# Kernel optimization log

Hardware: AMD Instinct MI355X
Metric: run time of the kernel (lower is better)

Reference implementation:

```python
import jax, jax.numpy as jnp
import numpy as np

B, S, D, NH, HFF, VOCAB = 128, 100, 512, 8, 2048, 50000
DH = D // NH
GH, GL, NC = 256, 2, 10  # GRU hidden, GRU layers, num classes
NE = 3  # num encoders


def setup_inputs() -> dict:
    key = jax.random.key(0)
    ks = jax.random.split(key, 32)
    f = lambda k, shp, s=0.02: (jax.random.normal(k, shp, dtype=jnp.float32) * s)
    inp = {
        'x': jax.random.randint(ks[0], (B, S), 0, VOCAB),
        'x1': jnp.ones((B, S), dtype=jnp.float32),
        'emb': f(ks[1], (VOCAB, D)),
        'Wq': f(ks[2], (NE, D, D)), 'bq': jnp.zeros((NE, D)),
        'Wk': f(ks[3], (NE, D, D)), 'bk': jnp.zeros((NE, D)),
        'Wv': f(ks[4], (NE, D, D)), 'bv': jnp.zeros((NE, D)),
        'Wo': f(ks[5], (NE, D, D)), 'bo': jnp.zeros((NE, D)),
        'g1': jnp.ones((NE, D)), 'be1': jnp.zeros((NE, D)),
        'W1': f(ks[6], (NE, D, HFF)), 'b1': jnp.zeros((NE, HFF)),
        'W2': f(ks[7], (NE, HFF, D)), 'b2': jnp.zeros((NE, D)),
        'g2': jnp.ones((NE, D)), 'be2': jnp.zeros((NE, D)),
        'gru_Wih': f(ks[8], (GL, 2, 3 * GH, D)),
        'gru_Whh': f(ks[9], (GL, 2, 3 * GH, GH)),
        'gru_bih': jnp.zeros((GL, 2, 3 * GH)),
        'gru_bhh': jnp.zeros((GL, 2, 3 * GH)),
        'fc_W': f(ks[10], (2 * GH + D, NC)), 'fc_b': jnp.zeros((NC,)),
    }
    return inp


def _layer_norm(x, g, b, eps=1e-5):
    m = jnp.mean(x, axis=-1, keepdims=True)
    v = jnp.mean((x - m) ** 2, axis=-1, keepdims=True)
    return (x - m) / jnp.sqrt(v + eps) * g + b


def _forward(x, emb, Wq, bq, Wk, bk, Wv, bv, Wo, bo, g1, be1, W1, b1, W2, b2,
             g2, be2, gru_Wih, gru_Whh, gru_bih, gru_bhh, fc_W, fc_b):
    out = emb[x]  # [B, S, D]
    scale = DH ** -0.5
    for l in range(NE):
        # NOTE: torch code uses a contiguous view(B*NH, -1, DH), not a
        # transpose-based head split; plain reshape reproduces it exactly.
        Q = (out @ Wq[l] + bq[l]).reshape(B * NH, S, DH)
        K = (out @ Wk[l] + bk[l]).reshape(B * NH, S, DH)
        V = (out @ Wv[l] + bv[l]).reshape(B * NH, S, DH)
        att = jax.nn.softmax(jnp.einsum('bqd,bkd->bqk', Q, K) * scale, axis=-1)
        ctx = (att @ V).reshape(B, S, D)
        out = _layer_norm(ctx @ Wo[l] + bo[l] + out, g1[l], be1[l])
        ff = jnp.maximum(out @ W1[l] + b1[l], 0.0) @ W2[l] + b2[l]
        out = _layer_norm(ff + out, g2[l], be2[l])
    embed_feat = out

    # Bidirectional multi-layer GRU (torch cuDNN formulation), seq-major.
    h_seq = jnp.transpose(out, (1, 0, 2))  # [S, B, D]
    for l in range(GL):
        dirs = []
        for d in range(2):
            Wih, Whh = gru_Wih[l, d], gru_Whh[l, d]
            bih, bhh = gru_bih[l, d], gru_bhh[l, d]
            xp = h_seq @ Wih.T + bih  # [S, B, 3H]

            def step(h, xpt, Whh=Whh, bhh=bhh):
                hp = h @ Whh.T + bhh
                r = jax.nn.sigmoid(xpt[:, :GH] + hp[:, :GH])
                z = jax.nn.sigmoid(xpt[:, GH:2 * GH] + hp[:, GH:2 * GH])
                n = jnp.tanh(xpt[:, 2 * GH:] + r * hp[:, 2 * GH:])
                hn = (1.0 - z) * n + z * h
                return hn, hn

            h0 = jnp.zeros((B, GH), dtype=h_seq.dtype)
            _, ys = jax.lax.scan(step, h0, xp, reverse=(d == 1))
            dirs.append(ys)
        h_seq = jnp.concatenate(dirs, axis=-1)  # [S, B, 2H]
    gru_out = jnp.transpose(h_seq, (1, 0, 2))  # [B, S, 2H]

    feat = jnp.maximum(jnp.concatenate([embed_feat, gru_out], axis=-1), 0.0)
    pooled = jnp.max(feat, axis=1)  # MaxPool1d(pad_size) over seq -> [B, 2H+D]
    return pooled @ fc_W + fc_b


def reference(x, x1, emb, Wq, bq, Wk, bk, Wv, bv, Wo, bo, g1, be1, W1, b1,
              W2, b2, g2, be2, gru_Wih, gru_Whh, gru_bih, gru_bhh, fc_W, fc_b):
    # x1 (mask) is dead in the original module: the masked attention result is
    # immediately overwritten by the unmasked call, so it does not affect output.
    return _forward(x, emb, Wq, bq, Wk, bk, Wv, bv, Wo, bo, g1, be1, W1, b1,
                    W2, b2, g2, be2, gru_Wih, gru_Whh, gru_bih, gru_bhh,
                    fc_W, fc_b)
```

## Files before the change

kernel.cpp:

```cpp
#include <hip/hip_runtime.h>
#include <cstdint>

typedef __bf16 bf16x8 __attribute__((ext_vector_type(8)));
typedef float f32x4 __attribute__((ext_vector_type(4)));
typedef unsigned short ushort8 __attribute__((ext_vector_type(8)));

#define DEV __device__ __forceinline__
#define MFMA16(a, b, c) __builtin_amdgcn_mfma_f32_16x16x32_bf16((a), (b), (c), 0, 0, 0)
#define MFMA_AG(acc, hf, wf) \
  asm("v_mfma_f32_16x16x32_bf16 %0, %1, %2, %0" : "+v"(acc) : "v"(hf), "a"(wf))

DEV unsigned short f2b(float x) {
  union { float f; unsigned int u; } c; c.f = x;
  unsigned int u = c.u + 0x7fffu + ((c.u >> 16) & 1u);
  return (unsigned short)(u >> 16);
}
DEV float b2f(unsigned short x) {
  union { unsigned int u; float f; } c; c.u = ((unsigned int)x) << 16;
  return c.f;
}
DEV void gld_lds16(const void* g, void* l) {
  __builtin_amdgcn_global_load_lds(
      (const __attribute__((address_space(1))) unsigned int*)(uintptr_t)g,
      (__attribute__((address_space(3))) unsigned int*)(uintptr_t)l, 16, 0, 0);
}

__global__ __launch_bounds__(256) void convT_k(const float* __restrict__ in,
                                               unsigned short* __restrict__ out,
                                               int K, int N) {
  __shared__ float tile[64][65];
  int k0 = blockIdx.x * 64, n0 = blockIdx.y * 64;
  int wv = threadIdx.x >> 6, ln = threadIdx.x & 63;
  #pragma unroll
  for (int i = 0; i < 16; ++i) {
    int r = wv * 16 + i;
    tile[r][ln] = in[(size_t)(k0 + r) * N + (n0 + ln)];
  }
  __syncthreads();
  #pragma unroll
  for (int i = 0; i < 16; ++i) {
    int r = wv * 16 + i;
    out[(size_t)(n0 + r) * K + (k0 + ln)] = f2b(tile[ln][r]);
  }
}

__global__ void convB_k(const float* __restrict__ in, unsigned short* __restrict__ out, int n) {
  int stride = gridDim.x * blockDim.x;
  for (int i = blockIdx.x * blockDim.x + threadIdx.x; i < n; i += stride)
    out[i] = f2b(in[i]);
}

__global__ __launch_bounds__(256) void biasC_k(const float* __restrict__ bih,
                                               const float* __restrict__ bhh,
                                               float* __restrict__ cb) {
  int i = blockIdx.x * 256 + threadIdx.x;
  if (i < 4 * 768) {
    int c = i % 768;
    cb[i] = bih[i] + (c < 512 ? bhh[i] : 0.f);
  }
}

__global__ __launch_bounds__(256) void embed_k(const int* __restrict__ x, const float* __restrict__ emb,
                                               float* __restrict__ cf, unsigned short* __restrict__ cb) {
  int row = blockIdx.x * 4 + (threadIdx.x >> 6);
  int lane = threadIdx.x & 63;
  int tok = x[row];
  const float4* src = (const float4*)(emb + (size_t)tok * 512 + lane * 8);
  float4 a = src[0], b = src[1];
  float4* dst = (float4*)(cf + (size_t)row * 512 + lane * 8);
  dst[0] = a; dst[1] = b;
  ushort8 pk;
  pk[0] = f2b(a.x); pk[1] = f2b(a.y); pk[2] = f2b(a.z); pk[3] = f2b(a.w);
  pk[4] = f2b(b.x); pk[5] = f2b(b.y); pk[6] = f2b(b.z); pk[7] = f2b(b.w);
  *(ushort8*)(cb + (size_t)row * 512 + lane * 8) = pk;
}

DEV void stage_tile(const unsigned short* g, int ld, unsigned short* lds, int lane, int wave) {
  #pragma unroll
  for (int i = 0; i < 2; ++i) {
    int r0 = (i * 4 + wave) * 16;
    const unsigned short* src = g + (size_t)(r0 + (lane >> 2)) * ld + (lane & 3) * 8;
    gld_lds16(src, lds + r0 * 32);
  }
}

template <int RELU, int RES, int OF32, int OB16>
__global__ __launch_bounds__(256) void gemm_k(
    const unsigned short* __restrict__ A, const unsigned short* __restrict__ BT,
    const float* __restrict__ bias, const float* __restrict__ res,
    float* __restrict__ Cf, unsigned short* __restrict__ Cb,
    int M, int N, int K) {
  __shared__ unsigned short sA[2][128 * 32];
  __shared__ unsigned short sB[2][128 * 32];
  int tid = threadIdx.x, lane = tid & 63, wave = tid >> 6;
  int m0 = blockIdx.x * 128, n0 = blockIdx.y * 128;
  int lm = lane & 15, lk = (lane >> 4) * 8;
  int wr = wave >> 1, wc = wave & 1;
  f32x4 acc[4][4];
  #pragma unroll
  for (int i = 0; i < 4; ++i)
    #pragma unroll
    for (int j = 0; j < 4; ++j) acc[i][j] = (f32x4){0.f, 0.f, 0.f, 0.f};
  const unsigned short* Ab = A + (size_t)m0 * K;
  const unsigned short* Bb = BT + (size_t)n0 * K;
  int nk = K >> 5;
  stage_tile(Ab, K, sA[0], lane, wave);
  stage_tile(Bb, K, sB[0], lane, wave);
  __syncthreads();
  int buf = 0;
  for (int t = 0; t < nk; ++t) {
    if (t + 1 < nk) {
      stage_tile(Ab + (t + 1) * 32, K, sA[buf ^ 1], lane, wave);
      stage_tile(Bb + (t + 1) * 32, K, sB[buf ^ 1], lane, wave);
    }
    bf16x8 aF[4], bF[4];
    #pragma unroll
    for (int i = 0; i < 4; ++i) aF[i] = *(const bf16x8*)&sA[buf][(wr * 64 + i * 16 + lm) * 32 + lk];
    #pragma unroll
    for (int j = 0; j < 4; ++j) bF[j] = *(const bf16x8*)&sB[buf][(wc * 64 + j * 16 + lm) * 32 + lk];
    #pragma unroll
    for (int i = 0; i < 4; ++i)
      #pragma unroll
      for (int j = 0; j < 4; ++j) acc[i][j] = MFMA16(aF[i], bF[j], acc[i][j]);
    __syncthreads();
    buf ^= 1;
  }
  #pragma unroll
  for (int i = 0; i < 4; ++i) {
    int gr0 = m0 + wr * 64 + i * 16 + (lane >> 4) * 4;
    #pragma unroll
    for (int j = 0; j < 4; ++j) {
      int gc = n0 + wc * 64 + j * 16 + lm;
      float bv = bias[gc];
      #pragma unroll
      for (int q = 0; q < 4; ++q) {
        size_t idx = (size_t)(gr0 + q) * N + gc;
        float v = acc[i][j][q] + bv;
        if (RES) v += res[idx];
        if (RELU) v = fmaxf(v, 0.f);
        if (OF32) Cf[idx] = v;
        if (OB16) Cb[idx] = f2b(v);
      }
    }
  }
}

__global__ __launch_bounds__(256) void attn_k(const unsigned short* __restrict__ Q,
                                              const unsigned short* __restrict__ Kv,
                                              const unsigned short* __restrict__ V,
                                              unsigned short* __restrict__ ctx) {
  __shared__ unsigned short Ks[112 * 64];
  __shared__ unsigned short VT[64 * 128];
  __shared__ unsigned short Ps[112 * 128];
  int g = blockIdx.x;
  size_t base = (size_t)g * 6400;
  int tid = threadIdx.x, lane = tid & 63, wave = tid >> 6;
  int lm = lane & 15, lg = lane >> 4, lk = lg * 8;
  for (int idx = tid; idx < 112 * 8; idx += 256) {
    int row = idx >> 3, c8 = (idx & 7) * 8;
    int rr = row < 100 ? row : 99;
    *(ushort8*)&Ks[row * 64 + c8] = *(const ushort8*)&Kv[base + (size_t)rr * 64 + c8];
  }
  for (int idx = tid; idx < 64 * 28; idx += 256) { int c = idx / 28, j = idx % 28; VT[c * 128 + 100 + j] = 0; }
  for (int idx = tid; idx < 112 * 16; idx += 256) { int r = idx / 16, c = idx % 16; Ps[r * 128 + 112 + c] = 0; }
  for (int idx = tid; idx < 6400; idx += 256) {
    int c = idx / 100, j = idx % 100;
    VT[c * 128 + j] = V[base + (size_t)j * 64 + c];
  }
  __syncthreads();
  for (int rt = wave; rt < 7; rt += 4) {
    int arow = rt * 16 + lm;
    int qrow = arow < 100 ? arow : 99;
    bf16x8 aF0 = *(const bf16x8*)&Q[base + (size_t)qrow * 64 + lk];
    bf16x8 aF1 = *(const bf16x8*)&Q[base + (size_t)qrow * 64 + 32 + lk];
    f32x4 sc[7];
    #pragma unroll
    for (int ct = 0; ct < 7; ++ct) {
      bf16x8 b0 = *(const bf16x8*)&Ks[(ct * 16 + lm) * 64 + lk];
      bf16x8 b1 = *(const bf16x8*)&Ks[(ct * 16 + lm) * 64 + 32 + lk];
      f32x4 a = {0.f, 0.f, 0.f, 0.f};
      a = MFMA16(aF0, b0, a);
      a = MFMA16(aF1, b1, a);
      sc[ct] = a;
    }
    #pragma unroll
    for (int q = 0; q < 4; ++q) {
      float mx = -1e30f;
      #pragma unroll
      for (int ct = 0; ct < 7; ++ct) {
        int col = ct * 16 + lm;
        float v = sc[ct][q] * 0.125f;
        if (col < 100) mx = fmaxf(mx, v);
      }
      for (int off = 1; off < 16; off <<= 1) mx = fmaxf(mx, __shfl_xor(mx, off));
      float sum = 0.f; float pv[7];
      #pragma unroll
      for (int ct = 0; ct < 7; ++ct) {
        int col = ct * 16 + lm;
        float e = (col < 100) ? __expf(sc[ct][q] * 0.125f - mx) : 0.f;
        pv[ct] = e; sum += e;
      }
      for (int off = 1; off < 16; off <<= 1) sum += __shfl_xor(sum, off);
      float inv = 1.f / sum;
      int prow = rt * 16 + lg * 4 + q;
      #pragma unroll
      for (int ct = 0; ct < 7; ++ct) Ps[prow * 128 + ct * 16 + lm] = f2b(pv[ct] * inv);
    }
  }
  __syncthreads();
  for (int rt = wave; rt < 7; rt += 4) {
    bf16x8 aP[4];
    #pragma unroll
    for (int kc = 0; kc < 4; ++kc) aP[kc] = *(const bf16x8*)&Ps[(rt * 16 + lm) * 128 + kc * 32 + lk];
    #pragma unroll
    for (int ctp = 0; ctp < 4; ++ctp) {
      f32x4 o = {0.f, 0.f, 0.f, 0.f};
      #pragma unroll
      for (int kc = 0; kc < 4; ++kc) {
        bf16x8 bV = *(const bf16x8*)&VT[(ctp * 16 + lm) * 128 + kc * 32 + lk];
        o = MFMA16(aP[kc], bV, o);
      }
      #pragma unroll
      for (int q = 0; q < 4; ++q) {
        int ri = rt * 16 + lg * 4 + q;
        if (ri < 100) ctx[base + (size_t)ri * 64 + ctp * 16 + lm] = f2b(o[q]);
      }
    }
  }
}

__global__ __launch_bounds__(256) void ln_k(const float* __restrict__ in, const float* __restrict__ gamma,
                                            const float* __restrict__ beta, float* __restrict__ outF,
                                            unsigned short* __restrict__ outB) {
  int row = blockIdx.x * 4 + (threadIdx.x >> 6);
  int lane = threadIdx.x & 63;
  const float* p = in + (size_t)row * 512 + lane * 8;
  float4 v0 = *(const float4*)p;
  float4 v1 = *(const float4*)(p + 4);
  float x[8] = {v0.x, v0.y, v0.z, v0.w, v1.x, v1.y, v1.z, v1.w};
  float s = 0.f;
  #pragma unroll
  for (int e = 0; e < 8; ++e) s += x[e];
  #pragma unroll
  for (int off = 1; off < 64; off <<= 1) s += __shfl_xor(s, off);
  float mean = s * (1.f / 512.f);
  float vs = 0.f;
  #pragma unroll
  for (int e = 0; e < 8; ++e) { float d = x[e] - mean; vs += d * d; }
  #pragma unroll
  for (int off = 1; off < 64; off <<= 1) vs += __shfl_xor(vs, off);
  float rstd = rsqrtf(vs * (1.f / 512.f) + 1e-5f);
  int c0 = lane * 8;
  ushort8 pk;
  #pragma unroll
  for (int e = 0; e < 8; ++e) {
    float y = (x[e] - mean) * rstd * gamma[c0 + e] + beta[c0 + e];
    x[e] = y; pk[e] = f2b(y);
  }
  float4* po = (float4*)(outF + (size_t)row * 512 + c0);
  po[0] = make_float4(x[0], x[1], x[2], x[3]);
  po[1] = make_float4(x[4], x[5], x[6], x[7]);
  *(ushort8*)(outB + (size_t)row * 512 + c0) = pk;
}

__global__ __launch_bounds__(128) void seqT_k(const unsigned short* __restrict__ in,
                                              unsigned short* __restrict__ out) {
  int o = blockIdx.x;
  int s = o >> 7, b = o & 127;
  const uint2* src = (const uint2*)(in + (size_t)(b * 100 + s) * 512);
  uint2* dst = (uint2*)(out + (size_t)o * 512);
  dst[threadIdx.x] = src[threadIdx.x];
}

__global__ __launch_bounds__(512) __attribute__((amdgpu_waves_per_eu(2, 2))) void gru_k(
    const unsigned short* __restrict__ WhhB,
    const float* __restrict__ bhh,
    const float* __restrict__ xp,
    unsigned short* __restrict__ hout)
{
  __shared__ unsigned short hb[2][16 * 256];
  __shared__ char ldsn[131072];
  const int dir = blockIdx.x >> 3, bsl = blockIdx.x & 7;
  const int tid = threadIdx.x, lane = tid & 63, w = tid >> 6;
  const int lm = lane & 15, lg = lane >> 4, lk = lg * 8;
  const int col = w * 32 + lm;

  for (int i = tid; i < 16 * 256; i += 512) hb[0][i] = 0;

  {
    const unsigned short* wn = WhhB + (size_t)(dir * 768 + 512) * 256;
    #pragma unroll
    for (int ct = 0; ct < 2; ++ct)
      #pragma unroll
      for (int kt = 0; kt < 8; ++kt) {
        const unsigned short* src = wn + (size_t)(w * 32 + lm + ct * 16) * 256 + kt * 32 + lk;
        gld_lds16(src, ldsn + ((w * 2 + ct) * 8 + kt) * 1024);
      }
  }

  bf16x8 wr[2][8], wz[2][8];
  #pragma unroll
  for (int ct = 0; ct < 2; ++ct) {
    const unsigned short* wpr = WhhB + (size_t)(dir * 768 + col + ct * 16) * 256;
    const unsigned short* wpz = WhhB + (size_t)(dir * 768 + 256 + col + ct * 16) * 256;
    #pragma unroll
    for (int kt = 0; kt < 8; ++kt) {
      wr[ct][kt] = *(const bf16x8*)&wpr[kt * 32 + lk];
      wz[ct][kt] = *(const bf16x8*)&wpz[kt * 32 + lk];
    }
  }
  #pragma unroll
  for (int ct = 0; ct < 2; ++ct)
    #pragma unroll
    for (int kt = 0; kt < 8; ++kt) {
      asm("" : "+a"(wr[ct][kt]));
      asm("" : "+a"(wz[ct][kt]));
    }

  float bh2[2];
  bh2[0] = bhh[dir * 768 + 512 + col];
  bh2[1] = bhh[dir * 768 + 512 + col + 16];
  float hprev[2][4] = {{0.f, 0.f, 0.f, 0.f}, {0.f, 0.f, 0.f, 0.f}};

  const int s0 = dir ? 99 : 0, sstep = dir ? -1 : 1;
  unsigned short* hob = hout + ((size_t)(s0 * 128 + bsl * 16 + lg * 4)) * 512 + dir * 256 + col;
  const ptrdiff_t hstep = (ptrdiff_t)sstep * 65536;
  const float* xpb = xp + ((size_t)dir * 100 + s0) * 98304 + (size_t)(bsl * 16 + lg * 4) * 768 + col;
  const ptrdiff_t xstep = (ptrdiff_t)sstep * 98304;

  __syncthreads();

  const int swz = (lm & 7) << 4;
  const char* nbase = ldsn + w * 16384 + lane * 16;
  for (int t = 0; t < 100; ++t) {
    const int cur = t & 1;
    float xv[3][2][4];
    #pragma unroll
    for (int g = 0; g < 3; ++g)
      #pragma unroll
      for (int ct = 0; ct < 2; ++ct)
        #pragma unroll
        for (int q = 0; q < 4; ++q)
          xv[g][ct][q] = xpb[q * 768 + g * 256 + ct * 16];
    f32x4 aR0 = {0.f, 0.f, 0.f, 0.f}, aR1 = {0.f, 0.f, 0.f, 0.f};
    f32x4 aZ0 = {0.f, 0.f, 0.f, 0.f}, aZ1 = {0.f, 0.f, 0.f, 0.f};
    f32x4 aN0 = {0.f, 0.f, 0.f, 0.f}, aN1 = {0.f, 0.f, 0.f, 0.f};
    const char* hbase = (const char*)&hb[cur][0] + lm * 512;
    #pragma unroll
    for (int kt = 0; kt < 8; ++kt) {
      bf16x8 hF = *(const bf16x8*)(hbase + ((kt * 64 + lg * 16) ^ swz));
      MFMA_AG(aR0, hF, wr[0][kt]);
      MFMA_AG(aR1, hF, wr[1][kt]);
      MFMA_AG(aZ0, hF, wz[0][kt]);
      MFMA_AG(aZ1, hF, wz[1][kt]);
      bf16x8 n0 = *(const bf16x8*)(nbase + kt * 1024);
      bf16x8 n1 = *(const bf16x8*)(nbase + 8192 + kt * 1024);
      aN0 = MFMA16(hF, n0, aN0);
      aN1 = MFMA16(hF, n1, aN1);
    }
    #pragma unroll
    for (int ct = 0; ct < 2; ++ct) {
      f32x4 aR = ct ? aR1 : aR0;
      f32x4 aZ = ct ? aZ1 : aZ0;
      f32x4 aN = ct ? aN1 : aN0;
      #pragma unroll
      for (int q = 0; q < 4; ++q) {
        const int row = lg * 4 + q;
        const int hoff = (w * 64 + ct * 32 + lm * 2) ^ ((row & 7) << 4);
        float r = 1.f / (1.f + __expf(-(xv[0][ct][q] + aR[q])));
        float z = 1.f / (1.f + __expf(-(xv[1][ct][q] + aZ[q])));
        float nb = xv[2][ct][q] + r * (aN[q] + bh2[ct]);
        float n = 1.f - 2.f / (__expf(2.f * nb) + 1.f);
        float hn = (1.f - z) * n + z * hprev[ct][q];
        hprev[ct][q] = hn;
        unsigned short hbits = f2b(hn);
        *(unsigned short*)((char*)&hb[cur ^ 1][0] + row * 512 + hoff) = hbits;
        hob[q * 512 + ct * 16] = hbits;
      }
    }
    asm volatile("s_waitcnt lgkmcnt(0)" ::: "memory");
    __builtin_amdgcn_s_barrier();
    hob += hstep;
    xpb += xstep;
  }
}

__global__ __launch_bounds__(256) void pool_k(const float* __restrict__ ef, const unsigned short* __restrict__ h2,
                                              float* __restrict__ pooled) {
  int b = blockIdx.x, tid = threadIdx.x;
  for (int c = tid; c < 1024; c += 256) {
    float m = 0.f;
    if (c < 512) {
      for (int s = 0; s < 100; ++s) m = fmaxf(m, ef[((size_t)b * 100 + s) * 512 + c]);
    } else {
      int cc = c - 512;
      for (int s = 0; s < 100; ++s) m = fmaxf(m, b2f(h2[((size_t)s * 128 + b) * 512 + cc]));
    }
    pooled[b * 1024 + c] = m;
  }
}

__global__ __launch_bounds__(64) void fc_k(const float* __restrict__ pooled, const float* __restrict__ W,
                                           const float* __restrict__ bias, float* __restrict__ out) {
  int b = blockIdx.x, lane = threadIdx.x;
  float a[10];
  #pragma unroll
  for (int n = 0; n < 10; ++n) a[n] = 0.f;
  for (int k = lane; k < 1024; k += 64) {
    float pv = pooled[b * 1024 + k];
    const float* wr = W + k * 10;
    #pragma unroll
    for (int n = 0; n < 10; ++n) a[n] += pv * wr[n];
  }
  #pragma unroll
  for (int n = 0; n < 10; ++n)
    for (int off = 32; off > 0; off >>= 1) a[n] += __shfl_xor(a[n], off);
  if (lane == 0) {
    #pragma unroll
    for (int n = 0; n < 10; ++n) out[b * 10 + n] = a[n] + bias[n];
  }
}

extern "C" void kernel_launch(void* const* d_in, const int* in_sizes, int n_in,
                              void* d_out, int out_size, void* d_ws, size_t ws_size,
                              hipStream_t stream) {
  (void)in_sizes; (void)n_in; (void)out_size;
  const int*   x   = (const int*)d_in[0];
  const float* emb = (const float*)d_in[2];
  const float* Wq  = (const float*)d_in[3];  const float* bq  = (const float*)d_in[4];
  const float* Wk  = (const float*)d_in[5];  const float* bk  = (const float*)d_in[6];
  const float* Wv  = (const float*)d_in[7];  const float* bv  = (const float*)d_in[8];
  const float* Wo  = (const float*)d_in[9];  const float* bo  = (const float*)d_in[10];
  const float* g1  = (const float*)d_in[11]; const float* be1 = (const float*)d_in[12];
  const float* W1  = (const float*)d_in[13]; const float* b1  = (const float*)d_in[14];
  const float* W2  = (const float*)d_in[15]; const float* b2  = (const float*)d_in[16];
  const float* g2  = (const float*)d_in[17]; const float* be2 = (const float*)d_in[18];
  const float* Wih = (const float*)d_in[19]; const float* Whh = (const float*)d_in[20];
  const float* bih = (const float*)d_in[21]; const float* bhh = (const float*)d_in[22];
  const float* fcW = (const float*)d_in[23]; const float* fcb = (const float*)d_in[24];

  if (ws_size < 193986560ULL) return;
  char* ws = (char*)d_ws;

  const size_t O_CURF = 0, O_CURBF = 26214400, O_WQT = 39321600, O_WKT = 40894464,
               O_WVT = 42467328, O_WOT = 44040192, O_W1T = 45613056, O_W2T = 51904512,
               O_WIH = 58195968, O_WHH = 61341696, O_A = 62914560;
  float* cur_f = (float*)(ws + O_CURF);
  unsigned short* cur_bf = (unsigned short*)(ws + O_CURBF);
  unsigned short* WqT = (unsigned short*)(ws + O_WQT);
  unsigned short* WkT = (unsigned short*)(ws + O_WKT);
  unsigned short* WvT = (unsigned short*)(ws + O_WVT);
  unsigned short* WoT = (unsigned short*)(ws + O_WOT);
  unsigned short* W1T = (unsigned short*)(ws + O_W1T);
  unsigned short* W2T = (unsigned short*)(ws + O_W2T);
  unsigned short* WihB = (unsigned short*)(ws + O_WIH);
  unsigned short* WhhB = (unsigned short*)(ws + O_WHH);
  float* cbias = (float*)(ws + O_WQT);
  unsigned short* Qb  = (unsigned short*)(ws + O_A);
  unsigned short* Kb  = (unsigned short*)(ws + O_A + 13107200);
  unsigned short* Vb  = (unsigned short*)(ws + O_A + 26214400);
  unsigned short* ctx = (unsigned short*)(ws + O_A + 39321600);
  unsigned short* ff1 = (unsigned short*)(ws + O_A + 52428800);
  float* tmp_f = (float*)(ws + O_A + 104857600);
  unsigned short* xseq  = (unsigned short*)(ws + O_A);
  float* xp             = (float*)(ws + O_A + 13107200);
  unsigned short* hout1 = (unsigned short*)(ws + O_A + 91750400);
  unsigned short* hout2 = (unsigned short*)(ws + O_A + 104857600);
  float* pooled         = (float*)(ws + O_A + 117964800);

  for (int l = 0; l < 3; ++l) {
    convT_k<<<dim3(8, 8), 256, 0, stream>>>(Wq + (size_t)l * 262144, WqT + (size_t)l * 262144, 512, 512);
    convT_k<<<dim3(8, 8), 256, 0, stream>>>(Wk + (size_t)l * 262144, WkT + (size_t)l * 262144, 512, 512);
    convT_k<<<dim3(8, 8), 256, 0, stream>>>(Wv + (size_t)l * 262144, WvT + (size_t)l * 262144, 512, 512);
    convT_k<<<dim3(8, 8), 256, 0, stream>>>(Wo + (size_t)l * 262144, WoT + (size_t)l * 262144, 512, 512);
    convT_k<<<dim3(8, 32), 256, 0, stream>>>(W1 + (size_t)l * 1048576, W1T + (size_t)l * 1048576, 512, 2048);
    convT_k<<<dim3(32, 8), 256, 0, stream>>>(W2 + (size_t)l * 1048576, W2T + (size_t)l * 1048576, 2048, 512);
  }
  convB_k<<<1024, 256, 0, stream>>>(Wih, WihB, 2 * 2 * 768 * 512);
  convB_k<<<512, 256, 0, stream>>>(Whh, WhhB, 2 * 2 * 768 * 256);

  embed_k<<<3200, 256, 0, stream>>>(x, emb, cur_f, cur_bf);

  for (int l = 0; l < 3; ++l) {
    gemm_k<0, 0, 0, 1><<<dim3(100, 4), 256, 0, stream>>>(cur_bf, WqT + (size_t)l * 262144, bq + l * 512, nullptr, nullptr, Qb, 12800, 512, 512);
    gemm_k<0, 0, 0, 1><<<dim3(100, 4), 256, 0, stream>>>(cur_bf, WkT + (size_t)l * 262144, bk + l * 512, nullptr, nullptr, Kb, 12800, 512, 512);
    gemm_k<0, 0, 0, 1><<<dim3(100, 4), 256, 0, stream>>>(cur_bf, WvT + (size_t)l * 262144, bv + l * 512, nullptr, nullptr, Vb, 12800, 512, 512);
    attn_k<<<1024, 256, 0, stream>>>(Qb, Kb, Vb, ctx);
    gemm_k<0, 1, 1, 0><<<dim3(100, 4), 256, 0, stream>>>(ctx, WoT + (size_t)l * 262144, bo + l * 512, cur_f, tmp_f, nullptr, 12800, 512, 512);
    ln_k<<<3200, 256, 0, stream>>>(tmp_f, g1 + l * 512, be1 + l * 512, cur_f, cur_bf);
    gemm_k<1, 0, 0, 1><<<dim3(100, 16), 256, 0, stream>>>(cur_bf, W1T + (size_t)l * 1048576, b1 + l * 2048, nullptr, nullptr, ff1, 12800, 2048, 512);
    gemm_k<0, 1, 1, 0><<<dim3(100, 4), 256, 0, stream>>>(ff1, W2T + (size_t)l * 1048576, b2 + l * 512, cur_f, tmp_f, nullptr, 12800, 512, 2048);
    ln_k<<<3200, 256, 0, stream>>>(tmp_f, g2 + l * 512, be2 + l * 512, cur_f, cur_bf);
  }

  biasC_k<<<12, 256, 0, stream>>>(bih, bhh, cbias);
  seqT_k<<<12800, 128, 0, stream>>>(cur_bf, xseq);
  for (int l = 0; l < 2; ++l) {
    const unsigned short* Ain = (l == 0) ? xseq : hout1;
    for (int d = 0; d < 2; ++d)
      gemm_k<0, 0, 1, 0><<<dim3(100, 6), 256, 0, stream>>>(
          Ain, WihB + ((size_t)l * 2 + d) * 768 * 512, cbias + (l * 2 + d) * 768, nullptr,
          xp + (size_t)d * 9830400, nullptr, 12800, 768, 512);
    gru_k<<<16, 512, 0, stream>>>(WhhB + (size_t)l * 2 * 768 * 256, bhh + l * 2 * 768, xp,
                                  (l == 0) ? hout1 : hout2);
  }

  pool_k<<<128, 256, 0, stream>>>(cur_f, hout2, pooled);
  fc_k<<<128, 64, 0, stream>>>(pooled, fcW, fcb, (float*)d_out);
}
```

Measured before the change: 1.403 ms.

## Halve GRU block to 4 waves, each computing 64 hidden columns

```diff
diff --git a/kernel.cpp b/kernel.cpp
--- a/kernel.cpp
+++ b/kernel.cpp
@@ -272,7 +272,7 @@
   dst[threadIdx.x] = src[threadIdx.x];
 }
 
-__global__ __launch_bounds__(512) __attribute__((amdgpu_waves_per_eu(2, 2))) void gru_k(
+__global__ __launch_bounds__(256) __attribute__((amdgpu_waves_per_eu(1, 1))) void gru_k(
     const unsigned short* __restrict__ WhhB,
     const float* __restrict__ bhh,
     const float* __restrict__ xp,
@@ -283,26 +283,25 @@
   const int dir = blockIdx.x >> 3, bsl = blockIdx.x & 7;
   const int tid = threadIdx.x, lane = tid & 63, w = tid >> 6;
   const int lm = lane & 15, lg = lane >> 4, lk = lg * 8;
-  const int col = w * 32 + lm;
-
-  for (int i = tid; i < 16 * 256; i += 512) hb[0][i] = 0;
+
+  for (int i = tid; i < 16 * 256; i += 256) hb[0][i] = 0;
 
   {
     const unsigned short* wn = WhhB + (size_t)(dir * 768 + 512) * 256;
     #pragma unroll
-    for (int ct = 0; ct < 2; ++ct)
+    for (int ct = 0; ct < 4; ++ct)
       #pragma unroll
       for (int kt = 0; kt < 8; ++kt) {
-        const unsigned short* src = wn + (size_t)(w * 32 + lm + ct * 16) * 256 + kt * 32 + lk;
-        gld_lds16(src, ldsn + ((w * 2 + ct) * 8 + kt) * 1024);
-      }
-  }
-
-  bf16x8 wr[2][8], wz[2][8];
-  #pragma unroll
-  for (int ct = 0; ct < 2; ++ct) {
-    const unsigned short* wpr = WhhB + (size_t)(dir * 768 + col + ct * 16) * 256;
-    const unsigned short* wpz = WhhB + (size_t)(dir * 768 + 256 + col + ct * 16) * 256;
+        const unsigned short* src = wn + (size_t)(w * 64 + ct * 16 + lm) * 256 + kt * 32 + lk;
+        gld_lds16(src, ldsn + (size_t)w * 32768 + (ct * 8 + kt) * 1024);
+      }
+  }
+
+  bf16x8 wr[4][8], wz[4][8];
+  #pragma unroll
+  for (int ct = 0; ct < 4; ++ct) {
+    const unsigned short* wpr = WhhB + (size_t)(dir * 768 + w * 64 + ct * 16 + lm) * 256;
+    const unsigned short* wpz = WhhB + (size_t)(dir * 768 + 256 + w * 64 + ct * 16 + lm) * 256;
     #pragma unroll
     for (int kt = 0; kt < 8; ++kt) {
       wr[ct][kt] = *(const bf16x8*)&wpr[kt * 32 + lk];
@@ -310,67 +309,80 @@
     }
   }
   #pragma unroll
-  for (int ct = 0; ct < 2; ++ct)
+  for (int ct = 0; ct < 4; ++ct)
     #pragma unroll
     for (int kt = 0; kt < 8; ++kt) {
       asm("" : "+a"(wr[ct][kt]));
       asm("" : "+a"(wz[ct][kt]));
     }
 
-  float bh2[2];
-  bh2[0] = bhh[dir * 768 + 512 + col];
-  bh2[1] = bhh[dir * 768 + 512 + col + 16];
-  float hprev[2][4] = {{0.f, 0.f, 0.f, 0.f}, {0.f, 0.f, 0.f, 0.f}};
+  float bh2[4];
+  #pragma unroll
+  for (int ct = 0; ct < 4; ++ct) bh2[ct] = bhh[dir * 768 + 512 + w * 64 + ct * 16 + lm];
+  float hprev[4][4];
+  #pragma unroll
+  for (int ct = 0; ct < 4; ++ct)
+    #pragma unroll
+    for (int q = 0; q < 4; ++q) hprev[ct][q] = 0.f;
 
   const int s0 = dir ? 99 : 0, sstep = dir ? -1 : 1;
-  unsigned short* hob = hout + ((size_t)(s0 * 128 + bsl * 16 + lg * 4)) * 512 + dir * 256 + col;
+  unsigned short* hob = hout + ((size_t)(s0 * 128 + bsl * 16 + lg * 4)) * 512 + dir * 256 + w * 64 + lm;
   const ptrdiff_t hstep = (ptrdiff_t)sstep * 65536;
-  const float* xpb = xp + ((size_t)dir * 100 + s0) * 98304 + (size_t)(bsl * 16 + lg * 4) * 768 + col;
+  const float* xpb = xp + ((size_t)dir * 100 + s0) * 98304 + (size_t)(bsl * 16 + lg * 4) * 768 + w * 64 + lm;
   const ptrdiff_t xstep = (ptrdiff_t)sstep * 98304;
 
   __syncthreads();
 
   const int swz = (lm & 7) << 4;
-  const char* nbase = ldsn + w * 16384 + lane * 16;
+  const char* nb = ldsn + (size_t)w * 32768 + lane * 16;
   for (int t = 0; t < 100; ++t) {
     const int cur = t & 1;
-    float xv[3][2][4];
+    float xv[3][4][4];
     #pragma unroll
     for (int g = 0; g < 3; ++g)
       #pragma unroll
-      for (int ct = 0; ct < 2; ++ct)
+      for (int ct = 0; ct < 4; ++ct)
         #pragma unroll
         for (int q = 0; q < 4; ++q)
           xv[g][ct][q] = xpb[q * 768 + g * 256 + ct * 16];
-    f32x4 aR0 = {0.f, 0.f, 0.f, 0.f}, aR1 = {0.f, 0.f, 0.f, 0.f};
-    f32x4 aZ0 = {0.f, 0.f, 0.f, 0.f}, aZ1 = {0.f, 0.f, 0.f, 0.f};
-    f32x4 aN0 = {0.f, 0.f, 0.f, 0.f}, aN1 = {0.f, 0.f, 0.f, 0.f};
     const char* hbase = (const char*)&hb[cur][0] + lm * 512;
+    bf16x8 hF[8];
+    #pragma unroll
+    for (int kt = 0; kt < 8; ++kt)
+      hF[kt] = *(const bf16x8*)(hbase + ((kt * 64 + lg * 16) ^ swz));
+    f32x4 aR[4], aZ[4], aN[4];
+    #pragma unroll
+    for (int ct = 0; ct < 4; ++ct) {
+      aR[ct] = (f32x4){0.f, 0.f, 0.f, 0.f};
+      aZ[ct] = (f32x4){0.f, 0.f, 0.f, 0.f};
+      aN[ct] = (f32x4){0.f, 0.f, 0.f, 0.f};
+    }
     #pragma unroll
     for (int kt = 0; kt < 8; ++kt) {
-      bf16x8 hF = *(const bf16x8*)(hbase + ((kt * 64 + lg * 16) ^ swz));
-      MFMA_AG(aR0, hF, wr[0][kt]);
-      MFMA_AG(aR1, hF, wr[1][kt]);
-      MFMA_AG(aZ0, hF, wz[0][kt]);
-      MFMA_AG(aZ1, hF, wz[1][kt]);
-      bf16x8 n0 = *(const bf16x8*)(nbase + kt * 1024);
-      bf16x8 n1 = *(const bf16x8*)(nbase + 8192 + kt * 1024);
-      aN0 = MFMA16(hF, n0, aN0);
-      aN1 = MFMA16(hF, n1, aN1);
-    }
-    #pragma unroll
-    for (int ct = 0; ct < 2; ++ct) {
-      f32x4 aR = ct ? aR1 : aR0;
-      f32x4 aZ = ct ? aZ1 : aZ0;
-      f32x4 aN = ct ? aN1 : aN0;
+      bf16x8 n0 = *(const bf16x8*)(nb + (0 * 8 + kt) * 1024);
+      bf16x8 n1 = *(const bf16x8*)(nb + (1 * 8 + kt) * 1024);
+      bf16x8 n2 = *(const bf16x8*)(nb + (2 * 8 + kt) * 1024);
+      bf16x8 n3 = *(const bf16x8*)(nb + (3 * 8 + kt) * 1024);
+      #pragma unroll
+      for (int ct = 0; ct < 4; ++ct) {
+        MFMA_AG(aR[ct], hF[kt], wr[ct][kt]);
+        MFMA_AG(aZ[ct], hF[kt], wz[ct][kt]);
+      }
+      aN[0] = MFMA16(hF[kt], n0, aN[0]);
+      aN[1] = MFMA16(hF[kt], n1, aN[1]);
+      aN[2] = MFMA16(hF[kt], n2, aN[2]);
+      aN[3] = MFMA16(hF[kt], n3, aN[3]);
+    }
+    #pragma unroll
+    for (int ct = 0; ct < 4; ++ct) {
       #pragma unroll
       for (int q = 0; q < 4; ++q) {
         const int row = lg * 4 + q;
-        const int hoff = (w * 64 + ct * 32 + lm * 2) ^ ((row & 7) << 4);
-        float r = 1.f / (1.f + __expf(-(xv[0][ct][q] + aR[q])));
-        float z = 1.f / (1.f + __expf(-(xv[1][ct][q] + aZ[q])));
-        float nb = xv[2][ct][q] + r * (aN[q] + bh2[ct]);
-        float n = 1.f - 2.f / (__expf(2.f * nb) + 1.f);
+        const int hoff = (w * 128 + ct * 32 + lm * 2) ^ ((row & 7) << 4);
+        float r = 1.f / (1.f + __expf(-(xv[0][ct][q] + aR[ct][q])));
+        float z = 1.f / (1.f + __expf(-(xv[1][ct][q] + aZ[ct][q])));
+        float nbv = xv[2][ct][q] + r * (aN[ct][q] + bh2[ct]);
+        float n = 1.f - 2.f / (__expf(2.f * nbv) + 1.f);
         float hn = (1.f - z) * n + z * hprev[ct][q];
         hprev[ct][q] = hn;
         unsigned short hbits = f2b(hn);
@@ -501,7 +513,7 @@
       gemm_k<0, 0, 1, 0><<<dim3(100, 6), 256, 0, stream>>>(
           Ain, WihB + ((size_t)l * 2 + d) * 768 * 512, cbias + (l * 2 + d) * 768, nullptr,
           xp + (size_t)d * 9830400, nullptr, 12800, 768, 512);
-    gru_k<<<16, 512, 0, stream>>>(WhhB + (size_t)l * 2 * 768 * 256, bhh + l * 2 * 768, xp,
+    gru_k<<<16, 256, 0, stream>>>(WhhB + (size_t)l * 2 * 768 * 256, bhh + l * 2 * 768, xp,
                                   (l == 0) ? hout1 : hout2);
   }
 
```

New measurement: 1.513 ms. 7.9% more time.
